# Kernel tuning notes

Measured on AMD Instinct MI355X. Metric: run time of the kernel, lower is better.

## Reference

```python
import jax, jax.numpy as jnp
import numpy as np

TAU = 0.6      # init_tau (membrane decay, also scales surrogate h_t)
TAU_O = 0.6    # init_tau_o (output / eligibility kappa filter)
THR = 0.6      # init_thresh (spike threshold)
LR = 0.05      # e-prop grad accumulation factor


def setup_inputs() -> dict:
    key = jax.random.key(0)
    k0, k1, k2, k3, k4 = jax.random.split(key, 5)
    B, T, NI, NH, NO = 64, 100, 700, 512, 20
    # binary spike inputs / one-hot-ish labels (rand -> threshold keeps SNN semantics)
    x = (jax.random.uniform(k0, (B, T, NI)) < 0.3).astype(jnp.float32)
    label = (jax.random.uniform(k1, (B, T, NO)) < 0.5).astype(jnp.float32)
    # kaiming_normal_ then *0.5 for fc1/out; kaiming_normal_ for recurrent
    w_fc1 = jax.random.normal(k2, (NH, NI), jnp.float32) * (0.5 * np.sqrt(2.0 / NI))
    w_rec = jax.random.normal(k3, (NH, NH), jnp.float32) * np.sqrt(2.0 / NH)
    w_out = jax.random.normal(k4, (NO, NH), jnp.float32) * (0.5 * np.sqrt(2.0 / NH))
    return dict(x=x, label=label, training=1, w_fc1=w_fc1, w_rec=w_rec, w_out=w_out)


def reference(x, label, training, w_fc1, w_rec, w_out):
    B, T, NI = x.shape
    NH = w_fc1.shape[0]
    NO = w_out.shape[0]
    dt = x.dtype

    def step(carry, xs):
        (hm, hs, om, os, tin, trec, tout, ein, erec, prev_hs, gf, gr, go) = carry
        xt, lt = xs  # [B,NI], [B,NO]
        # LIF hidden: decay (with reset-by-spike) + input + recurrent
        hidden_input = xt @ w_fc1.T + hs @ w_rec
        hm = TAU * hm * (1.0 - hs) + hidden_input
        hs = (hm >= THR).astype(dt)
        # LIF output
        om = TAU * om * (1.0 - os) + hs @ w_out.T
        os = (om >= THR).astype(dt)
        err = os - lt
        # surrogate derivative (triangle)
        h_t = TAU * jnp.maximum(0.0, 1.0 - jnp.abs((hm - THR) / THR))
        # presynaptic traces (trace_rec uses z_{t-1})
        tin = TAU * tin + xt
        trec = TAU * trec + prev_hs
        # eligibility traces: per-sample outer products, kappa-filtered
        ein = TAU_O * ein + h_t[:, :, None] * tin[:, None, :]    # [B,NH,NI]
        erec = TAU_O * erec + h_t[:, :, None] * trec[:, None, :]  # [B,NH,NH]
        tout = TAU_O * tout + hs
        # learning signal broadcast from output error
        L = err @ w_out  # [B,NH]
        gf = gf + LR * jnp.einsum('br,bri->ri', L, ein)
        gr = gr + LR * jnp.einsum('br,brj->rj', L, erec)
        go = go + LR * jnp.einsum('bo,br->or', err, tout)
        return (hm, hs, om, os, tin, trec, tout, ein, erec, hs, gf, gr, go), os

    z = lambda *s: jnp.zeros(s, dt)
    carry0 = (z(B, NH), z(B, NH), z(B, NO), z(B, NO), z(B, NI), z(B, NH),
              z(B, NH), z(B, NH, NI), z(B, NH, NH), z(B, NH),
              z(NH, NI), z(NH, NH), z(NO, NH))
    xs = (jnp.swapaxes(x, 0, 1), jnp.swapaxes(label, 0, 1))  # time-major
    carryF, outs = jax.lax.scan(step, carry0, xs)
    outputs = jnp.swapaxes(outs, 0, 1)  # [B,T,NO]
    return outputs, carryF[10], carryF[11], carryF[12]
```

## Files before the change

kernel.cpp:

```cpp
#include <hip/hip_runtime.h>
#include <hip/hip_bf16.h>

constexpr int kB  = 64;
constexpr int kT  = 100;
constexpr int kNI = 700;
constexpr int kNH = 512;
constexpr int kNO = 20;
constexpr float TAU   = 0.6f;
constexpr float TAU_O = 0.6f;
constexpr float THR   = 0.6f;
constexpr float LR    = 0.05f;

constexpr size_t BNH = (size_t)kB * kNH;
constexpr size_t BNI = (size_t)kB * kNI;
constexpr size_t BNO = (size_t)kB * kNO;
constexpr int kK   = kT * kB;
constexpr int kKP  = 704;

typedef __attribute__((ext_vector_type(8))) short short8;
typedef __attribute__((ext_vector_type(4))) float f32x4;

constexpr size_t O_XW   = 0;
constexpr size_t O_PGF  = 0;
constexpr size_t O_PGR  = 1572864;
constexpr size_t O_PGO  = 2621440;
constexpr size_t O_HSUR = 3276800;
constexpr size_t O_ERR  = 6553600;
constexpr size_t O_MTB  = 6681600;
constexpr size_t O_TRB  = 8320000;
constexpr size_t O_MSK  = 9958400;
constexpr size_t O_TIB  = 10060800;
constexpr size_t O_CNT  = 12300800;
constexpr size_t WS_FLOATS = 12300864;

constexpr size_t OUT_GF = (size_t)kB * kT * kNO;
constexpr size_t OUT_GR = OUT_GF + (size_t)kNH * kNI;
constexpr size_t OUT_GO = OUT_GR + (size_t)kNH * kNH;

__global__ __launch_bounds__(256) void k_xw2(const float* __restrict__ x,
                                             const float* __restrict__ wfc,
                                             float* __restrict__ XW) {
    int bx = blockIdx.x;
    int mt = bx % 50, nt = bx / 50;
    int m0 = mt * 128, n0 = nt * 64;
    int tid = threadIdx.x, tx = tid & 15, ty = tid >> 4;
    __shared__ float As[128][20];
    __shared__ float Bs[16][64];
    float acc[8][4] = {};
    int arow = tid >> 1, ahalf = tid & 1;
    int bb = (m0 + arow) & 63, tt = (m0 + arow) >> 6;
    const float* ap = x + ((size_t)bb * kT + tt) * kNI;
    int br = tid >> 2, bc4 = tid & 3;
    const float* wp = wfc + (size_t)(n0 + br) * kNI;
    for (int k0 = 0; k0 < kKP; k0 += 16) {
        #pragma unroll
        for (int u = 0; u < 2; u++) {
            int k = k0 + ahalf * 8 + u * 4;
            float4 v = (k + 3 < kNI) ? *(const float4*)(ap + k)
                                     : make_float4(0.f, 0.f, 0.f, 0.f);
            *(float4*)&As[arow][ahalf * 8 + u * 4] = v;
        }
        {
            int k = k0 + bc4 * 4;
            float4 v = (k + 3 < kNI) ? *(const float4*)(wp + k)
                                     : make_float4(0.f, 0.f, 0.f, 0.f);
            Bs[bc4 * 4 + 0][br] = v.x; Bs[bc4 * 4 + 1][br] = v.y;
            Bs[bc4 * 4 + 2][br] = v.z; Bs[bc4 * 4 + 3][br] = v.w;
        }
        __syncthreads();
        #pragma unroll
        for (int kk = 0; kk < 16; kk++) {
            float av[8];
            #pragma unroll
            for (int i = 0; i < 4; i++) {
                av[i]     = As[ty * 4 + i][kk];
                av[4 + i] = As[64 + ty * 4 + i][kk];
            }
            float4 b0 = *(const float4*)&Bs[kk][tx * 4];
            float bv[4] = {b0.x, b0.y, b0.z, b0.w};
            #pragma unroll
            for (int i = 0; i < 8; i++)
                #pragma unroll
                for (int j = 0; j < 4; j++) acc[i][j] += av[i] * bv[j];
        }
        __syncthreads();
    }
    #pragma unroll
    for (int i = 0; i < 8; i++) {
        int m = m0 + ((i < 4) ? (ty * 4 + i) : (64 + ty * 4 + i - 4));
        float* dst = XW + (size_t)m * kNH + n0;
        *(float4*)(dst + tx * 4) = make_float4(acc[i][0], acc[i][1], acc[i][2], acc[i][3]);
    }
}

__global__ __launch_bounds__(832) void k_forward(float* __restrict__ ws,
                                                 const float* __restrict__ label,
                                                 const float* __restrict__ w_rec,
                                                 const float* __restrict__ w_out,
                                                 float* __restrict__ dout,
                                                 unsigned long long* __restrict__ gmask,
                                                 const float* __restrict__ x) {
    __shared__ float wout_ld[kNO * kNH];
    __shared__ float partial[8][kNH];
    __shared__ unsigned long long mh[kT * 8];
    __shared__ float errh[kT * kNO];

    int bxg = blockIdx.x, tid = threadIdx.x;
    if (bxg >= kB) {
        int idx = (bxg - kB) * 832 + tid;
        if (idx < (int)BNI) {
            int b = idx / kNI, i = idx - b * kNI;
            const float* xp = x + (size_t)b * kT * kNI + i;
            unsigned short* tib = (unsigned short*)(ws + O_TIB);
            size_t rowoff = (size_t)i * kK + (size_t)b * 100;
            float v = 0.f;
            for (int tq = 0; tq < 25; tq++) {
                unsigned long long w8 = 0;
                #pragma unroll
                for (int u = 0; u < 4; u++) {
                    int t = tq * 4 + u;
                    v = TAU * v + xp[(size_t)t * kNI];
                    __hip_bfloat16 bv = __float2bfloat16(v);
                    w8 |= ((unsigned long long)*(unsigned short*)&bv) << (16 * u);
                }
                *(unsigned long long*)&tib[rowoff + tq * 4] = w8;
            }
        }
        return;
    }

    int b = bxg;
    int wave = tid >> 6, lane = tid & 63;
    const f32x4* wr4 = (const f32x4*)w_rec;
    for (int e = tid; e < kNO * kNH; e += 832) wout_ld[e] = w_out[e];
    float hm = 0.f, sp_prev = 0.f;
    float om_r[4] = {0.f, 0.f, 0.f, 0.f}, os_r[4] = {0.f, 0.f, 0.f, 0.f};
    int q = wave - 8;
    const int coff = lane * 2;
    __syncthreads();

    for (int t = 0; t < kT; t++) {
        float xw = 0.f;
        if (wave < 8) {
            xw = ws[O_XW + ((size_t)t * 64 + b) * kNH + tid];
            unsigned long long m = (t > 0) ? mh[(t - 1) * 8 + wave] : 0ull;
            const size_t base = (size_t)wave * 64;
            f32x4 s0 = {0.f, 0.f, 0.f, 0.f}, s1 = s0;
            while (m) {
                int j = __builtin_ctzll(m); m &= m - 1;
                const f32x4* r = wr4 + (base + j) * 128 + coff;
                s0 += r[0]; s1 += r[1];
            }
            *(f32x4*)&partial[wave][lane * 8]     = s0;
            *(f32x4*)&partial[wave][lane * 8 + 4] = s1;
        } else if (t > 0) {
            int to = t - 1;
            unsigned long long mk[8];
            #pragma unroll
            for (int k = 0; k < 8; k++) mk[k] = mh[to * 8 + k];
            #pragma unroll
            for (int r = 0; r < 4; r++) {
                int o = q * 4 + r;
                float p = 0.f;
                #pragma unroll
                for (int k = 0; k < 8; k++)
                    if ((mk[k] >> lane) & 1) p += wout_ld[o * kNH + 64 * k + lane];
                #pragma unroll
                for (int off = 32; off >= 1; off >>= 1) p += __shfl_xor(p, off);
                if (lane == 0) {
                    float om_n = TAU * om_r[r] * (1.f - os_r[r]) + p;
                    float os_n = (om_n >= THR) ? 1.f : 0.f;
                    om_r[r] = om_n; os_r[r] = os_n;
                    errh[to * kNO + o] = os_n - label[((size_t)b * kT + to) * kNO + o];
                    dout[((size_t)b * kT + to) * kNO + o] = os_n;
                }
            }
        }
        __syncthreads();
        if (tid < kNH) {
            float rec = ((partial[0][tid] + partial[1][tid]) + (partial[2][tid] + partial[3][tid]))
                      + ((partial[4][tid] + partial[5][tid]) + (partial[6][tid] + partial[7][tid]));
            hm = TAU * hm * (1.f - sp_prev) + (xw + rec);
            bool v = (hm >= THR);
            float sp = v ? 1.f : 0.f;
            sp_prev = sp;
            ws[O_HSUR + (size_t)t * BNH + (size_t)b * kNH + tid] =
                TAU * fmaxf(0.f, 1.f - fabsf(hm - THR) * (1.f / THR));
            unsigned long long bal = __ballot(v);
            if (lane == 0) {
                mh[t * 8 + wave] = bal;
                gmask[((size_t)t * 64 + b) * 8 + wave] = bal;
            }
        }
        __syncthreads();
    }
    if (wave >= 8) {
        int to = kT - 1;
        unsigned long long mk[8];
        #pragma unroll
        for (int k = 0; k < 8; k++) mk[k] = mh[to * 8 + k];
        #pragma unroll
        for (int r = 0; r < 4; r++) {
            int o = q * 4 + r;
            float p = 0.f;
            #pragma unroll
            for (int k = 0; k < 8; k++)
                if ((mk[k] >> lane) & 1) p += wout_ld[o * kNH + 64 * k + lane];
            #pragma unroll
            for (int off = 32; off >= 1; off >>= 1) p += __shfl_xor(p, off);
            if (lane == 0) {
                float om_n = TAU * om_r[r] * (1.f - os_r[r]) + p;
                float os_n = (om_n >= THR) ? 1.f : 0.f;
                errh[to * kNO + o] = os_n - label[((size_t)b * kT + to) * kNO + o];
                dout[((size_t)b * kT + to) * kNO + o] = os_n;
            }
        }
    }
    if (tid < kNH) {
        unsigned short* trb = (unsigned short*)(ws + O_TRB);
        size_t rowoff = (size_t)tid * kK + (size_t)b * 100;
        int w = tid >> 6, bit = tid & 63;
        float v = 0.f, p = 0.f;
        for (int tq = 0; tq < 25; tq++) {
            unsigned long long w8 = 0;
            #pragma unroll
            for (int u = 0; u < 4; u++) {
                int t = tq * 4 + u;
                v = TAU * v + p;
                __hip_bfloat16 bv = __float2bfloat16(v);
                w8 |= ((unsigned long long)*(unsigned short*)&bv) << (16 * u);
                p = (float)((mh[t * 8 + w] >> bit) & 1ull);
            }
            *(unsigned long long*)&trb[rowoff + tq * 4] = w8;
        }
    }
    __syncthreads();
    if (wave == 8 && lane < kNO) {
        float v = 0.f;
        for (int t = kT - 1; t >= 0; t--) {
            v = errh[t * kNO + lane] + TAU_O * v;
            errh[t * kNO + lane] = v;
            ws[O_ERR + (size_t)t * BNO + (size_t)b * kNO + lane] = v;
        }
    }
    __syncthreads();
    if (tid < kNH) {
        float wreg[kNO];
        #pragma unroll
        for (int o = 0; o < kNO; o++) wreg[o] = wout_ld[o * kNH + tid];
        unsigned short* mtb = (unsigned short*)(ws + O_MTB);
        size_t rowoff = (size_t)tid * kK + (size_t)b * 100;
        for (int tq = 0; tq < 25; tq++) {
            unsigned long long w8 = 0;
            #pragma unroll
            for (int u = 0; u < 4; u++) {
                int t = tq * 4 + u;
                float s = 0.f;
                #pragma unroll
                for (int o = 0; o < kNO; o++) s += errh[t * kNO + o] * wreg[o];
                float val = LR * s * ws[O_HSUR + (size_t)t * BNH + (size_t)b * kNH + tid];
                __hip_bfloat16 bv = __float2bfloat16(val);
                w8 |= ((unsigned long long)*(unsigned short*)&bv) << (16 * u);
            }
            *(unsigned long long*)&mtb[rowoff + tq * 4] = w8;
        }
    }
}

__global__ __launch_bounds__(256) void k_grads(float* __restrict__ ws,
                                               float* __restrict__ dout) {
    __shared__ unsigned short As[128 * 72];
    __shared__ unsigned short Bs[128 * 72];
    __shared__ int isLast;
    int bx = blockIdx.x, tid = threadIdx.x;
    int* cnt = (int*)(ws + O_CNT);

    if (bx < 160) {
        constexpr int KC = kK / 4, BK = 64, LDT = 72;
        const unsigned short* A = (const unsigned short*)(ws + O_MTB);
        const unsigned short* B;
        float* Cpart;
        int Nrows, ldc, s, mt, nt, tileid;
        if (bx < 96) {
            s = bx & 3; mt = (bx >> 2) & 3; nt = bx >> 4;
            B = (const unsigned short*)(ws + O_TIB);
            Cpart = ws + O_PGF; Nrows = kNI; ldc = 768;
            tileid = mt + 4 * nt;
        } else {
            int v = bx - 96;
            s = v & 3; mt = (v >> 2) & 3; nt = v >> 4;
            B = (const unsigned short*)(ws + O_TRB);
            Cpart = ws + O_PGR; Nrows = kNH; ldc = kNH;
            tileid = 24 + mt + 4 * nt;
        }
        int m0 = mt * 128, n0 = nt * 128, k0 = s * KC;
        int wave = tid >> 6, lane = tid & 63;
        int wm = wave & 1, wn = wave >> 1;
        f32x4 acc[4][4];
        #pragma unroll
        for (int i = 0; i < 4; i++)
            #pragma unroll
            for (int j = 0; j < 4; j++) acc[i][j] = (f32x4){0.f, 0.f, 0.f, 0.f};

        for (int kb = 0; kb < KC; kb += BK) {
            int kg = k0 + kb;
            #pragma unroll
            for (int p = 0; p < 4; p++) {
                int f = tid + p * 256;
                int row = f >> 3, seg = f & 7;
                *(short8*)&As[row * LDT + seg * 8] =
                    *(const short8*)&A[(size_t)(m0 + row) * kK + kg + seg * 8];
                short8 bv = {};
                if (n0 + row < Nrows)
                    bv = *(const short8*)&B[(size_t)(n0 + row) * kK + kg + seg * 8];
                *(short8*)&Bs[row * LDT + seg * 8] = bv;
            }
            __syncthreads();
            #pragma unroll
            for (int h = 0; h < 2; h++) {
                int kof = h * 32 + (lane >> 4) * 8;
                short8 af[4], bf[4];
                #pragma unroll
                for (int i = 0; i < 4; i++)
                    af[i] = *(short8*)&As[(wm * 64 + i * 16 + (lane & 15)) * LDT + kof];
                #pragma unroll
                for (int j = 0; j < 4; j++)
                    bf[j] = *(short8*)&Bs[(wn * 64 + j * 16 + (lane & 15)) * LDT + kof];
                #pragma unroll
                for (int i = 0; i < 4; i++)
                    #pragma unroll
                    for (int j = 0; j < 4; j++)
                        acc[i][j] = __builtin_amdgcn_mfma_f32_16x16x32_bf16(af[i], bf[j], acc[i][j], 0, 0, 0);
            }
            __syncthreads();
        }
        float* C = Cpart + (size_t)s * kNH * ldc;
        int rbase = (lane >> 4) * 4, col = lane & 15;
        #pragma unroll
        for (int i = 0; i < 4; i++)
            #pragma unroll
            for (int j = 0; j < 4; j++) {
                int n = n0 + wn * 64 + j * 16 + col;
                #pragma unroll
                for (int r = 0; r < 4; r++) {
                    int m = m0 + wm * 64 + i * 16 + rbase + r;
                    C[(size_t)m * ldc + n] = acc[i][j][r];
                }
            }
        __syncthreads();
        if (tid == 0)
            isLast = (__hip_atomic_fetch_add(&cnt[tileid], 1, __ATOMIC_ACQ_REL,
                                             __HIP_MEMORY_SCOPE_AGENT) == 3);
        __syncthreads();
        if (isLast) {
            if (bx < 96) {
                for (int e = tid; e < 128 * 128; e += 256) {
                    int m = m0 + (e >> 7), n = n0 + (e & 127);
                    if (n < kNI) {
                        float sv = 0.f;
                        size_t src = O_PGF + (size_t)m * 768 + n;
                        #pragma unroll
                        for (int k = 0; k < 4; k++) sv += ws[src + (size_t)k * kNH * 768];
                        dout[OUT_GF + (size_t)m * kNI + n] = sv;
                    }
                }
            } else {
                for (int e = tid; e < 128 * 128; e += 256) {
                    int m = m0 + (e >> 7), n = n0 + (e & 127);
                    float sv = 0.f;
                    size_t src = O_PGR + (size_t)m * kNH + n;
                    #pragma unroll
                    for (int k = 0; k < 4; k++) sv += ws[src + (size_t)k * kNH * kNH];
                    dout[OUT_GR + (size_t)m * kNH + n] = sv;
                }
            }
        }
    } else {
        float* Asf = (float*)As;
        float* Bsf = (float*)Bs;
        const float* A = ws + O_ERR;
        const unsigned long long* gm = (const unsigned long long*)(ws + O_MSK);
        int v = bx - 160;
        int s = v & 7, nt = v >> 3;
        int n0 = nt * 64, k0 = s * 800;
        int w0 = n0 >> 6;
        int tx = tid & 15, ty = tid >> 4;
        float acc[4][4] = {};
        for (int kb = 0; kb < 800; kb += 16) {
            #pragma unroll
            for (int e = tid; e < 1024; e += 256) {
                int kk = e >> 6, c = e & 63;
                size_t gk = (size_t)(k0 + kb + kk);
                Asf[kk * 64 + c] = (c < kNO) ? A[gk * kNO + c] : 0.f;
                Bsf[kk * 64 + c] = (float)((gm[gk * 8 + w0] >> c) & 1ull);
            }
            __syncthreads();
            #pragma unroll
            for (int kk = 0; kk < 16; kk++) {
                float4 av = *(const float4*)&Asf[kk * 64 + ty * 4];
                float4 bv = *(const float4*)&Bsf[kk * 64 + tx * 4];
                float aa[4] = {av.x, av.y, av.z, av.w};
                float bb[4] = {bv.x, bv.y, bv.z, bv.w};
                #pragma unroll
                for (int a = 0; a < 4; a++)
                    #pragma unroll
                    for (int c = 0; c < 4; c++) acc[a][c] += aa[a] * bb[c];
            }
            __syncthreads();
        }
        float* Cs = ws + O_PGO + (size_t)s * kNO * kNH;
        #pragma unroll
        for (int a = 0; a < 4; a++) {
            int m = ty * 4 + a;
            if (m < kNO) {
                #pragma unroll
                for (int c = 0; c < 4; c++)
                    Cs[(size_t)m * kNH + n0 + tx * 4 + c] = acc[a][c];
            }
        }
        __syncthreads();
        if (tid == 0)
            isLast = (__hip_atomic_fetch_add(&cnt[40 + nt], 1, __ATOMIC_ACQ_REL,
                                             __HIP_MEMORY_SCOPE_AGENT) == 7);
        __syncthreads();
        if (isLast) {
            for (int e = tid; e < kNO * 64; e += 256) {
                int o = e >> 6, c = e & 63;
                float sv = 0.f;
                size_t src = O_PGO + (size_t)o * kNH + n0 + c;
                #pragma unroll
                for (int k = 0; k < 8; k++) sv += ws[src + (size_t)k * kNO * kNH];
                dout[OUT_GO + (size_t)o * kNH + n0 + c] = LR * sv;
            }
        }
    }
}

extern "C" void kernel_launch(void* const* d_in, const int* in_sizes, int n_in,
                              void* d_out, int out_size, void* d_ws, size_t ws_size,
                              hipStream_t stream) {
    (void)in_sizes; (void)n_in; (void)out_size;
    const float* x     = (const float*)d_in[0];
    const float* label = (const float*)d_in[1];
    const float* w_fc1 = (const float*)d_in[3];
    const float* w_rec = (const float*)d_in[4];
    const float* w_out = (const float*)d_in[5];
    float* out = (float*)d_out;
    float* ws  = (float*)d_ws;

    if (ws_size < WS_FLOATS * sizeof(float)) return;

    unsigned long long* gmask = (unsigned long long*)(ws + O_MSK);

    hipMemsetAsync(ws + O_CNT, 0, 64 * sizeof(int), stream);

    k_xw2<<<400, 256, 0, stream>>>(x, w_fc1, ws + O_XW);

    k_forward<<<kB + 54, 832, 0, stream>>>(ws, label, w_rec, w_out, out, gmask, x);

    k_grads<<<224, 256, 0, stream>>>(ws, out);

}
```

Before: 608.7 us.

## Fuse input GEMM into forward kernel with per-row-tile flag handoff

Merges the x·W_fc1 GEMM kernel and the recurrent forward kernel into one launch. GEMM blocks publish a per-m-tile completion counter, and forward blocks spin-wait on the tile for the upcoming timesteps, so the sequential recurrence can start before the whole GEMM finishes. This removes a kernel boundary and overlaps the input projection with the recurrence. In exchange, GEMM blocks run at 832 threads with only 256 active, and the cross-block spin-waits need all producer blocks to be resident or scheduled ahead of the consumers.

Result: no change. 608.5 us (-0.0%).

```diff
diff --git a/kernel.cpp b/kernel.cpp
--- a/kernel.cpp
+++ b/kernel.cpp
@@ -31,83 +31,87 @@
 constexpr size_t O_MSK  = 9958400;
 constexpr size_t O_TIB  = 10060800;
 constexpr size_t O_CNT  = 12300800;
-constexpr size_t WS_FLOATS = 12300864;
+constexpr size_t WS_FLOATS = 12300928;
 
 constexpr size_t OUT_GF = (size_t)kB * kT * kNO;
 constexpr size_t OUT_GR = OUT_GF + (size_t)kNH * kNI;
 constexpr size_t OUT_GO = OUT_GR + (size_t)kNH * kNH;
 
-__global__ __launch_bounds__(256) void k_xw2(const float* __restrict__ x,
-                                             const float* __restrict__ wfc,
-                                             float* __restrict__ XW) {
-    int bx = blockIdx.x;
-    int mt = bx % 50, nt = bx / 50;
-    int m0 = mt * 128, n0 = nt * 64;
-    int tid = threadIdx.x, tx = tid & 15, ty = tid >> 4;
-    __shared__ float As[128][20];
-    __shared__ float Bs[16][64];
-    float acc[8][4] = {};
-    int arow = tid >> 1, ahalf = tid & 1;
-    int bb = (m0 + arow) & 63, tt = (m0 + arow) >> 6;
-    const float* ap = x + ((size_t)bb * kT + tt) * kNI;
-    int br = tid >> 2, bc4 = tid & 3;
-    const float* wp = wfc + (size_t)(n0 + br) * kNI;
-    for (int k0 = 0; k0 < kKP; k0 += 16) {
-        #pragma unroll
-        for (int u = 0; u < 2; u++) {
-            int k = k0 + ahalf * 8 + u * 4;
-            float4 v = (k + 3 < kNI) ? *(const float4*)(ap + k)
-                                     : make_float4(0.f, 0.f, 0.f, 0.f);
-            *(float4*)&As[arow][ahalf * 8 + u * 4] = v;
-        }
-        {
-            int k = k0 + bc4 * 4;
-            float4 v = (k + 3 < kNI) ? *(const float4*)(wp + k)
-                                     : make_float4(0.f, 0.f, 0.f, 0.f);
-            Bs[bc4 * 4 + 0][br] = v.x; Bs[bc4 * 4 + 1][br] = v.y;
-            Bs[bc4 * 4 + 2][br] = v.z; Bs[bc4 * 4 + 3][br] = v.w;
-        }
-        __syncthreads();
-        #pragma unroll
-        for (int kk = 0; kk < 16; kk++) {
-            float av[8];
-            #pragma unroll
-            for (int i = 0; i < 4; i++) {
-                av[i]     = As[ty * 4 + i][kk];
-                av[4 + i] = As[64 + ty * 4 + i][kk];
-            }
-            float4 b0 = *(const float4*)&Bs[kk][tx * 4];
-            float bv[4] = {b0.x, b0.y, b0.z, b0.w};
-            #pragma unroll
-            for (int i = 0; i < 8; i++)
-                #pragma unroll
-                for (int j = 0; j < 4; j++) acc[i][j] += av[i] * bv[j];
-        }
-        __syncthreads();
-    }
-    #pragma unroll
-    for (int i = 0; i < 8; i++) {
-        int m = m0 + ((i < 4) ? (ty * 4 + i) : (64 + ty * 4 + i - 4));
-        float* dst = XW + (size_t)m * kNH + n0;
-        *(float4*)(dst + tx * 4) = make_float4(acc[i][0], acc[i][1], acc[i][2], acc[i][3]);
-    }
-}
-
-__global__ __launch_bounds__(832) void k_forward(float* __restrict__ ws,
-                                                 const float* __restrict__ label,
-                                                 const float* __restrict__ w_rec,
-                                                 const float* __restrict__ w_out,
-                                                 float* __restrict__ dout,
-                                                 unsigned long long* __restrict__ gmask,
-                                                 const float* __restrict__ x) {
-    __shared__ float wout_ld[kNO * kNH];
-    __shared__ float partial[8][kNH];
-    __shared__ unsigned long long mh[kT * 8];
-    __shared__ float errh[kT * kNO];
-
-    int bxg = blockIdx.x, tid = threadIdx.x;
-    if (bxg >= kB) {
-        int idx = (bxg - kB) * 832 + tid;
+__global__ __launch_bounds__(832) void k_main(float* __restrict__ ws,
+                                              const float* __restrict__ label,
+                                              const float* __restrict__ w_rec,
+                                              const float* __restrict__ w_out,
+                                              float* __restrict__ dout,
+                                              unsigned long long* __restrict__ gmask,
+                                              const float* __restrict__ x,
+                                              const float* __restrict__ wfc) {
+    __shared__ __align__(16) char smem[71744];
+    int bx = blockIdx.x, tid = threadIdx.x;
+    int* cnt = (int*)(ws + O_CNT);
+
+    if (bx < 400) {
+        float* As = (float*)smem;
+        float* Bs = (float*)(smem + 40960);
+        int mt = bx >> 3, nt = bx & 7;
+        int m0 = mt * 128, n0 = nt * 64;
+        float acc[8][4] = {};
+        int tx = tid & 15, ty = (tid >> 4) & 15;
+        int arow = (tid >> 1) & 127, ahalf = tid & 1;
+        int bb = (m0 + arow) & 63, tt = (m0 + arow) >> 6;
+        const float* ap = x + ((size_t)bb * kT + tt) * kNI;
+        int br = (tid >> 2) & 63, bc4 = tid & 3;
+        const float* wp = wfc + (size_t)(n0 + br) * kNI;
+        for (int k0 = 0; k0 < kKP; k0 += 16) {
+            if (tid < 256) {
+                #pragma unroll
+                for (int u = 0; u < 2; u++) {
+                    int k = k0 + ahalf * 8 + u * 4;
+                    float4 v = (k + 3 < kNI) ? *(const float4*)(ap + k)
+                                             : make_float4(0.f, 0.f, 0.f, 0.f);
+                    *(float4*)&As[arow * 20 + ahalf * 8 + u * 4] = v;
+                }
+                int k = k0 + bc4 * 4;
+                float4 v = (k + 3 < kNI) ? *(const float4*)(wp + k)
+                                         : make_float4(0.f, 0.f, 0.f, 0.f);
+                Bs[(bc4 * 4 + 0) * 64 + br] = v.x; Bs[(bc4 * 4 + 1) * 64 + br] = v.y;
+                Bs[(bc4 * 4 + 2) * 64 + br] = v.z; Bs[(bc4 * 4 + 3) * 64 + br] = v.w;
+            }
+            __syncthreads();
+            if (tid < 256) {
+                #pragma unroll
+                for (int kk = 0; kk < 16; kk++) {
+                    float av[8];
+                    #pragma unroll
+                    for (int i = 0; i < 4; i++) {
+                        av[i]     = As[(ty * 4 + i) * 20 + kk];
+                        av[4 + i] = As[(64 + ty * 4 + i) * 20 + kk];
+                    }
+                    float4 b0 = *(const float4*)&Bs[kk * 64 + tx * 4];
+                    float bv[4] = {b0.x, b0.y, b0.z, b0.w};
+                    #pragma unroll
+                    for (int i = 0; i < 8; i++)
+                        #pragma unroll
+                        for (int j = 0; j < 4; j++) acc[i][j] += av[i] * bv[j];
+                }
+            }
+            __syncthreads();
+        }
+        if (tid < 256) {
+            #pragma unroll
+            for (int i = 0; i < 8; i++) {
+                int m = m0 + ((i < 4) ? (ty * 4 + i) : (64 + ty * 4 + i - 4));
+                float* dst = ws + O_XW + (size_t)m * kNH + n0;
+                *(float4*)(dst + tx * 4) = make_float4(acc[i][0], acc[i][1], acc[i][2], acc[i][3]);
+            }
+        }
+        __syncthreads();
+        if (tid == 0)
+            __hip_atomic_fetch_add(&cnt[mt], 1, __ATOMIC_ACQ_REL, __HIP_MEMORY_SCOPE_AGENT);
+        return;
+    }
+
+    if (bx >= 464) {
+        int idx = (bx - 464) * 832 + tid;
         if (idx < (int)BNI) {
             int b = idx / kNI, i = idx - b * kNI;
             const float* xp = x + (size_t)b * kT * kNI + i;
@@ -129,7 +133,12 @@
         return;
     }
 
-    int b = bxg;
+    float* wout_ld = (float*)smem;
+    float* partial = (float*)(smem + 40960);
+    unsigned long long* mh = (unsigned long long*)(smem + 57344);
+    float* errh = (float*)(smem + 63744);
+
+    int b = bx - 400;
     int wave = tid >> 6, lane = tid & 63;
     const f32x4* wr4 = (const f32x4*)w_rec;
     for (int e = tid; e < kNO * kNH; e += 832) wout_ld[e] = w_out[e];
@@ -137,6 +146,11 @@
     float om_r[4] = {0.f, 0.f, 0.f, 0.f}, os_r[4] = {0.f, 0.f, 0.f, 0.f};
     int q = wave - 8;
     const int coff = lane * 2;
+    int mtw = 0;
+    if (tid == 0) {
+        while (__hip_atomic_load(&cnt[0], __ATOMIC_RELAXED, __HIP_MEMORY_SCOPE_AGENT) < 8)
+            __builtin_amdgcn_s_sleep(8);
+    }
     __syncthreads();
 
     for (int t = 0; t < kT; t++) {
@@ -151,8 +165,8 @@
                 const f32x4* r = wr4 + (base + j) * 128 + coff;
                 s0 += r[0]; s1 += r[1];
             }
-            *(f32x4*)&partial[wave][lane * 8]     = s0;
-            *(f32x4*)&partial[wave][lane * 8 + 4] = s1;
+            *(f32x4*)&partial[wave * kNH + lane * 8]     = s0;
+            *(f32x4*)&partial[wave * kNH + lane * 8 + 4] = s1;
         } else if (t > 0) {
             int to = t - 1;
             unsigned long long mk[8];
@@ -178,8 +192,10 @@
         }
         __syncthreads();
         if (tid < kNH) {
-            float rec = ((partial[0][tid] + partial[1][tid]) + (partial[2][tid] + partial[3][tid]))
-                      + ((partial[4][tid] + partial[5][tid]) + (partial[6][tid] + partial[7][tid]));
+            float rec = ((partial[0 * kNH + tid] + partial[1 * kNH + tid]) +
+                         (partial[2 * kNH + tid] + partial[3 * kNH + tid])) +
+                        ((partial[4 * kNH + tid] + partial[5 * kNH + tid]) +
+                         (partial[6 * kNH + tid] + partial[7 * kNH + tid]));
             hm = TAU * hm * (1.f - sp_prev) + (xw + rec);
             bool v = (hm >= THR);
             float sp = v ? 1.f : 0.f;
@@ -190,6 +206,14 @@
             if (lane == 0) {
                 mh[t * 8 + wave] = bal;
                 gmask[((size_t)t * 64 + b) * 8 + wave] = bal;
+            }
+        }
+        if (tid == 0) {
+            int nmt = (t + 1) >> 1;
+            if (nmt > mtw && nmt < 50) {
+                while (__hip_atomic_load(&cnt[nmt], __ATOMIC_RELAXED, __HIP_MEMORY_SCOPE_AGENT) < 8)
+                    __builtin_amdgcn_s_sleep(8);
+                mtw = nmt;
             }
         }
         __syncthreads();
@@ -349,7 +373,7 @@
             }
         __syncthreads();
         if (tid == 0)
-            isLast = (__hip_atomic_fetch_add(&cnt[tileid], 1, __ATOMIC_ACQ_REL,
+            isLast = (__hip_atomic_fetch_add(&cnt[50 + tileid], 1, __ATOMIC_ACQ_REL,
                                              __HIP_MEMORY_SCOPE_AGENT) == 3);
         __syncthreads();
         if (isLast) {
@@ -420,7 +444,7 @@
         }
         __syncthreads();
         if (tid == 0)
-            isLast = (__hip_atomic_fetch_add(&cnt[40 + nt], 1, __ATOMIC_ACQ_REL,
+            isLast = (__hip_atomic_fetch_add(&cnt[90 + nt], 1, __ATOMIC_ACQ_REL,
                                              __HIP_MEMORY_SCOPE_AGENT) == 7);
         __syncthreads();
         if (isLast) {
@@ -452,12 +476,9 @@
 
     unsigned long long* gmask = (unsigned long long*)(ws + O_MSK);
 
-    hipMemsetAsync(ws + O_CNT, 0, 64 * sizeof(int), stream);
-
-    k_xw2<<<400, 256, 0, stream>>>(x, w_fc1, ws + O_XW);
-
-    k_forward<<<kB + 54, 832, 0, stream>>>(ws, label, w_rec, w_out, out, gmask, x);
+    hipMemsetAsync(ws + O_CNT, 0, 128 * sizeof(int), stream);
+
+    k_main<<<518, 832, 0, stream>>>(ws, label, w_rec, w_out, out, gmask, x, w_fc1);
 
     k_grads<<<224, 256, 0, stream>>>(ws, out);
-
 }
```
